# Kernel optimization log

Measured on AMD Instinct MI355X. Metric: run time of the kernel, lower is better.

Reference implementation:

```python
import jax, jax.numpy as jnp
import numpy as np

T = 2048      # tokens (flattened batch*seq)
HID = 2048    # hidden_size
H = 16        # num heads
D = HID // H  # head_dim = 128
EPS = 1e-5
THETA = 1000000.0


def setup_inputs() -> dict:
    key = jax.random.key(0)
    k0, k1, k2 = jax.random.split(key, 3)
    return {
        "hidden_states": jax.random.normal(k0, (T, HID), jnp.float32),
        "positions": jnp.arange(T, dtype=jnp.int32),
        "w_qkv": jax.random.normal(k1, (HID, 3 * HID), jnp.float32) * 0.02,
        "q_norm_w": jnp.ones((HID,), jnp.float32),
        "k_norm_w": jnp.ones((HID,), jnp.float32),
        "w_o": jax.random.normal(k2, (HID, HID), jnp.float32) * 0.02,
    }


def _rmsnorm(x, w):
    # RMSNorm over the full flat q/k vector (q_size / kv_size), as in forward_native
    var = jnp.mean(jnp.square(x.astype(jnp.float32)), axis=-1, keepdims=True)
    return (x.astype(jnp.float32) * jax.lax.rsqrt(var + EPS)).astype(x.dtype) * w


def _rope(x, positions):
    # NEOX-style rotary over full head_dim. x: [T, H, D]
    half = D // 2
    inv_freq = 1.0 / (THETA ** (jnp.arange(half, dtype=jnp.float32) / half))
    ang = positions.astype(jnp.float32)[:, None] * inv_freq  # [T, half]
    cos = jnp.cos(ang)[:, None, :]  # [T, 1, half]
    sin = jnp.sin(ang)[:, None, :]
    x1, x2 = x[..., :half], x[..., half:]
    return jnp.concatenate([x1 * cos - x2 * sin, x2 * cos + x1 * sin], axis=-1)


def reference(hidden_states, positions, w_qkv, q_norm_w, k_norm_w, w_o):
    qkv = hidden_states @ w_qkv                      # [T, 3*HID]
    q, k, v = jnp.split(qkv, [HID, 2 * HID], axis=-1)
    q = _rmsnorm(q, q_norm_w)
    k = _rmsnorm(k, k_norm_w)
    q = _rope(q.reshape(T, H, D), positions)
    k = _rope(k.reshape(T, H, D), positions)
    v = v.reshape(T, H, D)
    scale = D ** -0.5
    scores = jnp.einsum('qhd,khd->hqk', q, k) * scale   # [H, T, T]
    causal = jnp.tril(jnp.ones((T, T), bool))
    scores = jnp.where(causal[None], scores, jnp.finfo(scores.dtype).min)
    probs = jax.nn.softmax(scores, axis=-1)
    attn = jnp.einsum('hqk,khd->qhd', probs, v).reshape(T, HID)
    return attn @ w_o
```

## Files before the change

kernel.cpp:

```cpp
#include <hip/hip_runtime.h>
#include <hip/hip_bf16.h>

typedef __attribute__((ext_vector_type(8))) short bf16x8;
typedef __attribute__((ext_vector_type(4))) float f32x4;

__device__ inline unsigned short f2b(float x) {
  __hip_bfloat16 b = __float2bfloat16(x);
  return *reinterpret_cast<unsigned short*>(&b);
}
__device__ inline float b2f(unsigned short u) {
  return __bfloat162float(*reinterpret_cast<const __hip_bfloat16*>(&u));
}

#define GAS(p) ((const __attribute__((address_space(1))) void*)(p))
#define LAS(p) ((__attribute__((address_space(3))) void*)(p))

__global__ __launch_bounds__(256) void cast_f32_bf16(const float* __restrict__ X,
                                                     unsigned short* __restrict__ Y, int n4) {
  int i = blockIdx.x * 256 + threadIdx.x;
  if (i < n4) {
    float4 v = reinterpret_cast<const float4*>(X)[i];
    ushort4 o;
    o.x = f2b(v.x); o.y = f2b(v.y); o.z = f2b(v.z); o.w = f2b(v.w);
    reinterpret_cast<ushort4*>(Y)[i] = o;
  }
}

__global__ __launch_bounds__(256) void tcast(const float* __restrict__ W,
                                             unsigned short* __restrict__ Wt, int K, int N) {
  __shared__ float tile[32][33];
  int n0 = blockIdx.x * 32, k0 = blockIdx.y * 32;
  int tx = threadIdx.x & 31, ty = threadIdx.x >> 5;
#pragma unroll
  for (int i = 0; i < 32; i += 8)
    tile[ty + i][tx] = W[(size_t)(k0 + ty + i) * N + n0 + tx];
  __syncthreads();
#pragma unroll
  for (int i = 0; i < 32; i += 8)
    Wt[(size_t)(n0 + ty + i) * K + k0 + tx] = f2b(tile[tx][ty + i]);
}

__global__ __launch_bounds__(256) void vtrans(const float* __restrict__ qkv,
                                              unsigned short* __restrict__ Vt) {
  __shared__ unsigned short tile[32][33];
  int c0 = blockIdx.x * 32;
  int t0 = blockIdx.y * 32;
  int tx = threadIdx.x & 31, ty = threadIdx.x >> 5;
#pragma unroll
  for (int i = 0; i < 32; i += 8)
    tile[ty + i][tx] = f2b(qkv[(size_t)(t0 + ty + i) * 6144 + 4096 + c0 + tx]);
  __syncthreads();
#pragma unroll
  for (int i = 0; i < 32; i += 8)
    Vt[(size_t)(c0 + ty + i) * 2048 + t0 + tx] = tile[tx][ty + i];
}

__global__ __launch_bounds__(256) void gemm_bt(const unsigned short* __restrict__ A,
                                               const unsigned short* __restrict__ Bt,
                                               float* __restrict__ C, int M, int N, int K) {
  __shared__ unsigned short As[128 * 32];
  __shared__ unsigned short Bs[128 * 32];
  const int tid = threadIdx.x;
  const int w = tid >> 6, l = tid & 63;
  const int lr = l & 15, lg = l >> 4;
  const int wm = (w >> 1) << 6, wn = (w & 1) << 6;
  const size_t bm = (size_t)blockIdx.y * 128, bn = (size_t)blockIdx.x * 128;

  const int srow = tid >> 2;
  const int scol = (tid & 3) << 3;
  const unsigned short* Ag = A + (bm + srow) * (size_t)K + scol;
  const unsigned short* Bg = Bt + (bn + srow) * (size_t)K + scol;
  unsigned short* Al = As + w * 512;
  unsigned short* Bl = Bs + w * 512;

  f32x4 acc[4][4] = {};

  for (int k0 = 0; k0 < K; k0 += 32) {
    __syncthreads();
    __builtin_amdgcn_global_load_lds(GAS(Ag + k0), LAS(Al), 16, 0, 0);
    __builtin_amdgcn_global_load_lds(GAS(Ag + (size_t)64 * K + k0), LAS(Al + 2048), 16, 0, 0);
    __builtin_amdgcn_global_load_lds(GAS(Bg + k0), LAS(Bl), 16, 0, 0);
    __builtin_amdgcn_global_load_lds(GAS(Bg + (size_t)64 * K + k0), LAS(Bl + 2048), 16, 0, 0);
    __syncthreads();

    bf16x8 af[4], bfr[4];
#pragma unroll
    for (int mi = 0; mi < 4; ++mi)
      af[mi] = *reinterpret_cast<const bf16x8*>(&As[(wm + mi * 16 + lr) * 32 + lg * 8]);
#pragma unroll
    for (int ni = 0; ni < 4; ++ni)
      bfr[ni] = *reinterpret_cast<const bf16x8*>(&Bs[(wn + ni * 16 + lr) * 32 + lg * 8]);
#pragma unroll
    for (int mi = 0; mi < 4; ++mi)
#pragma unroll
      for (int ni = 0; ni < 4; ++ni)
        acc[mi][ni] = __builtin_amdgcn_mfma_f32_16x16x32_bf16(af[mi], bfr[ni], acc[mi][ni], 0, 0, 0);
  }

#pragma unroll
  for (int mi = 0; mi < 4; ++mi)
#pragma unroll
    for (int ni = 0; ni < 4; ++ni)
#pragma unroll
      for (int r = 0; r < 4; ++r) {
        size_t row = bm + wm + mi * 16 + lg * 4 + r;
        size_t col = bn + wn + ni * 16 + lr;
        C[row * N + col] = acc[mi][ni][r];
      }
}

__global__ __launch_bounds__(256) void rms_rope(const float* __restrict__ qkv,
                                                const int* __restrict__ pos,
                                                const float* __restrict__ qw,
                                                const float* __restrict__ kw,
                                                unsigned short* __restrict__ qb,
                                                unsigned short* __restrict__ kb) {
  const int t = blockIdx.x;
  const float* row = qkv + (size_t)t * 6144;
  __shared__ float redq[4], redk[4];
  __shared__ float cs[64], sn[64];
  const int tid = threadIdx.x, w = tid >> 6, l = tid & 63;

  float sq = 0.f, sk = 0.f;
#pragma unroll
  for (int i = 0; i < 8; ++i) {
    float a = row[tid + i * 256]; sq += a * a;
    float b = row[2048 + tid + i * 256]; sk += b * b;
  }
#pragma unroll
  for (int m = 32; m >= 1; m >>= 1) { sq += __shfl_xor(sq, m, 64); sk += __shfl_xor(sk, m, 64); }
  if (l == 0) { redq[w] = sq; redk[w] = sk; }
  if (tid < 64) {
    float fr = exp2f(-(float)tid * 0.31143075889569016f);
    float ang = (float)pos[t] * fr;
    cs[tid] = cosf(ang);
    sn[tid] = sinf(ang);
  }
  __syncthreads();
  float rq = rsqrtf((redq[0] + redq[1] + redq[2] + redq[3]) * (1.f / 2048.f) + 1e-5f);
  float rk = rsqrtf((redk[0] + redk[1] + redk[2] + redk[3]) * (1.f / 2048.f) + 1e-5f);

  unsigned short* qo = qb + (size_t)t * 2048;
  unsigned short* ko = kb + (size_t)t * 2048;
#pragma unroll
  for (int pp = 0; pp < 4; ++pp) {
    int pr = tid + pp * 256;
    int h = pr >> 6, j = pr & 63;
    int b0 = h * 128 + j;
    float c = cs[j], s = sn[j];
    float x1 = row[b0] * rq * qw[b0];
    float x2 = row[b0 + 64] * rq * qw[b0 + 64];
    qo[b0]      = f2b(x1 * c - x2 * s);
    qo[b0 + 64] = f2b(x2 * c + x1 * s);
    float y1 = row[2048 + b0] * rk * kw[b0];
    float y2 = row[2048 + b0 + 64] * rk * kw[b0 + 64];
    ko[b0]      = f2b(y1 * c - y2 * s);
    ko[b0 + 64] = f2b(y2 * c + y1 * s);
  }
}

__global__ __launch_bounds__(256) void attn_part(const unsigned short* __restrict__ qb,
                                                 const unsigned short* __restrict__ kb,
                                                 const unsigned short* __restrict__ vt,
                                                 unsigned short* __restrict__ Op,
                                                 float* __restrict__ ml) {
  __shared__ unsigned short Ks[64 * 128];
  __shared__ unsigned short Vs[128 * 64];
  __shared__ unsigned short Ps[4][16 * 72];
  const int qt = blockIdx.x, h = blockIdx.y, sp = blockIdx.z;
  const int q0 = qt * 64;
  const int kbeg = sp * 512;
  if (kbeg >= q0 + 64) return;
  const int kend = min(kbeg + 512, q0 + 64);
  const int tid = threadIdx.x, w = tid >> 6, l = tid & 63;
  const int lr = l & 15, lg = l >> 4;
  const float scale = 0.08838834764831845f;

  bf16x8 qf[4];
  {
    const unsigned short* qp = qb + (size_t)(q0 + w * 16 + lr) * 2048 + h * 128;
#pragma unroll
    for (int kc = 0; kc < 4; ++kc)
      qf[kc] = *reinterpret_cast<const bf16x8*>(qp + kc * 32 + lg * 8);
  }
  f32x4 oacc[8] = {};
  float mrow[4], lrow[4];
#pragma unroll
  for (int r = 0; r < 4; ++r) { mrow[r] = -1e30f; lrow[r] = 0.f; }

  for (int k0 = kbeg; k0 < kend; k0 += 64) {
    __syncthreads();
    {
      const int r0 = l >> 4, cph = l & 15;
#pragma unroll
      for (int rb = 0; rb < 16; rb += 4) {
        int row = w * 16 + rb + r0;
        int clog = (cph & 8) | ((cph & 7) ^ (row & 7));
        const unsigned short* src = kb + (size_t)(k0 + row) * 2048 + h * 128 + clog * 8;
        __builtin_amdgcn_global_load_lds(GAS(src), LAS((char*)Ks + (w * 16 + rb) * 256), 16, 0, 0);
      }
      const int r0v = l >> 3, cpv = l & 7;
#pragma unroll
      for (int rb = 0; rb < 32; rb += 8) {
        int row = w * 32 + rb + r0v;
        int clog = cpv ^ (row & 7);
        const unsigned short* src = vt + (size_t)(h * 128 + row) * 2048 + k0 + clog * 8;
        __builtin_amdgcn_global_load_lds(GAS(src), LAS((char*)Vs + (w * 32 + rb) * 128), 16, 0, 0);
      }
    }
    __syncthreads();

    f32x4 s[4] = {};
#pragma unroll
    for (int kc = 0; kc < 4; ++kc)
#pragma unroll
      for (int cg = 0; cg < 4; ++cg) {
        int key = cg * 16 + lr;
        int c = 4 * kc + lg;
        int cswz = (c & 8) | ((c & 7) ^ (key & 7));
        bf16x8 kf = *reinterpret_cast<const bf16x8*>(&Ks[key * 128 + cswz * 8]);
        s[cg] = __builtin_amdgcn_mfma_f32_16x16x32_bf16(qf[kc], kf, s[cg], 0, 0, 0);
      }

#pragma unroll
    for (int r = 0; r < 4; ++r) {
      const int qr = q0 + w * 16 + lg * 4 + r;
      float pv[4]; bool msk[4];
      float mx = -1e30f;
#pragma unroll
      for (int cg = 0; cg < 4; ++cg) {
        msk[cg] = (k0 + cg * 16 + lr) > qr;
        float v = msk[cg] ? -1e30f : s[cg][r] * scale;
        pv[cg] = v;
        mx = fmaxf(mx, v);
      }
#pragma unroll
      for (int m = 8; m >= 1; m >>= 1) mx = fmaxf(mx, __shfl_xor(mx, m, 16));
      float mnew = fmaxf(mrow[r], mx);
      float corr = __expf(mrow[r] - mnew);
      float ps = 0.f;
#pragma unroll
      for (int cg = 0; cg < 4; ++cg) {
        float pe = msk[cg] ? 0.f : __expf(pv[cg] - mnew);
        pv[cg] = pe; ps += pe;
      }
#pragma unroll
      for (int m = 8; m >= 1; m >>= 1) ps += __shfl_xor(ps, m, 16);
      lrow[r] = lrow[r] * corr + ps;
      mrow[r] = mnew;
#pragma unroll
      for (int ni = 0; ni < 8; ++ni) oacc[ni][r] *= corr;
#pragma unroll
      for (int cg = 0; cg < 4; ++cg)
        Ps[w][(lg * 4 + r) * 72 + cg * 16 + lr] = f2b(pv[cg]);
    }

#pragma unroll
    for (int ks = 0; ks < 2; ++ks) {
      bf16x8 pf = *reinterpret_cast<const bf16x8*>(&Ps[w][lr * 72 + ks * 32 + lg * 8]);
#pragma unroll
      for (int ni = 0; ni < 8; ++ni) {
        int d = ni * 16 + lr;
        int c = ks * 4 + lg;
        int cswz = c ^ (d & 7);
        bf16x8 vf = *reinterpret_cast<const bf16x8*>(&Vs[d * 64 + cswz * 8]);
        oacc[ni] = __builtin_amdgcn_mfma_f32_16x16x32_bf16(pf, vf, oacc[ni], 0, 0, 0);
      }
    }
  }

  const size_t base = (((size_t)sp * 16 + h) * 32 + qt) * 64;
#pragma unroll
  for (int ni = 0; ni < 8; ++ni)
#pragma unroll
    for (int r = 0; r < 4; ++r)
      Op[(base + w * 16 + lg * 4 + r) * 128 + ni * 16 + lr] = f2b(oacc[ni][r]);
  if (lr == 0) {
#pragma unroll
    for (int r = 0; r < 4; ++r) {
      size_t mi = (base + w * 16 + lg * 4 + r) * 2;
      ml[mi] = mrow[r]; ml[mi + 1] = lrow[r];
    }
  }
}

__global__ __launch_bounds__(256) void attn_combine(const unsigned short* __restrict__ Op,
                                                    const float* __restrict__ ml,
                                                    unsigned short* __restrict__ ob) {
  const int qt = blockIdx.x, h = blockIdx.y;
  const int q0 = qt * 64;
  const int ns = q0 / 512 + 1;
  const int t = threadIdx.x;
  const int row = t >> 2, dp = (t & 3) * 32;

  float m_s[4], l_s[4];
  float M = -1e30f;
#pragma unroll
  for (int s = 0; s < 4; ++s) {
    if (s < ns) {
      size_t mi = ((((size_t)s * 16 + h) * 32 + qt) * 64 + row) * 2;
      m_s[s] = ml[mi]; l_s[s] = ml[mi + 1];
    } else { m_s[s] = -1e30f; l_s[s] = 0.f; }
    M = fmaxf(M, m_s[s]);
  }
  float L = 0.f, wgt[4];
#pragma unroll
  for (int s = 0; s < 4; ++s) { wgt[s] = __expf(m_s[s] - M); L += l_s[s] * wgt[s]; }
  float invL = 1.f / L;

  float acc[32];
#pragma unroll
  for (int j = 0; j < 32; ++j) acc[j] = 0.f;
#pragma unroll
  for (int s = 0; s < 4; ++s) {
    if (s < ns) {
      const unsigned short* op = Op + ((((size_t)s * 16 + h) * 32 + qt) * 64 + row) * 128 + dp;
      float wg = wgt[s] * invL;
#pragma unroll
      for (int j = 0; j < 32; j += 8) {
        bf16x8 v = *reinterpret_cast<const bf16x8*>(op + j);
#pragma unroll
        for (int e = 0; e < 8; ++e) acc[j + e] += wg * b2f((unsigned short)v[e]);
      }
    }
  }
  unsigned short* o = ob + (size_t)(q0 + row) * 2048 + h * 128 + dp;
#pragma unroll
  for (int j = 0; j < 32; ++j) o[j] = f2b(acc[j]);
}

extern "C" void kernel_launch(void* const* d_in, const int* in_sizes, int n_in,
                              void* d_out, int out_size, void* d_ws, size_t ws_size,
                              hipStream_t stream) {
  const float* hs   = (const float*)d_in[0];
  const int*   pos  = (const int*)d_in[1];
  const float* wqkv = (const float*)d_in[2];
  const float* qnw  = (const float*)d_in[3];
  const float* knw  = (const float*)d_in[4];
  const float* wo   = (const float*)d_in[5];
  float* out = (float*)d_out;

  char* ws = (char*)d_ws;
  size_t off = 0;
  auto take = [&](size_t bytes) {
    char* p = ws + off;
    off = (off + bytes + 255) & ~(size_t)255;
    return p;
  };
  unsigned short* hidA  = (unsigned short*)take(2048ull * 2048 * 2);
  unsigned short* wqkvT = (unsigned short*)take(6144ull * 2048 * 2);
  unsigned short* woT   = (unsigned short*)take(2048ull * 2048 * 2);
  float*          qkvF  = (float*)take(2048ull * 6144 * 4);
  unsigned short* qbv   = (unsigned short*)take(2048ull * 2048 * 2);
  unsigned short* kbv   = (unsigned short*)take(2048ull * 2048 * 2);
  unsigned short* vtb   = (unsigned short*)take(2048ull * 2048 * 2);
  unsigned short* attnb = (unsigned short*)take(2048ull * 2048 * 2);
  unsigned short* Opart = (unsigned short*)qkvF;
  float*          mlb   = (float*)((char*)qkvF + 32ull * 1024 * 1024);

  cast_f32_bf16<<<4096, 256, 0, stream>>>(hs, hidA, 1048576);
  tcast<<<dim3(192, 64), 256, 0, stream>>>(wqkv, wqkvT, 2048, 6144);
  tcast<<<dim3(64, 64), 256, 0, stream>>>(wo, woT, 2048, 2048);
  gemm_bt<<<dim3(48, 16), 256, 0, stream>>>(hidA, wqkvT, qkvF, 2048, 6144, 2048);
  rms_rope<<<2048, 256, 0, stream>>>(qkvF, pos, qnw, knw, qbv, kbv);
  vtrans<<<dim3(64, 64), 256, 0, stream>>>(qkvF, vtb);
  attn_part<<<dim3(32, 16, 4), 256, 0, stream>>>(qbv, kbv, vtb, Opart, mlb);
  attn_combine<<<dim3(32, 16), 256, 0, stream>>>(Opart, mlb, attnb);
  gemm_bt<<<dim3(16, 16), 256, 0, stream>>>(attnb, woT, out, 2048, 2048, 2048);
}
```

Baseline: 362.6 us.

## Split attention KV into finer chunks, skip masking on full tiles, fold scale into Q

The KV split length drops from 512 to 256, giving eight splits, and partial outputs are packed into a compact triangular layout so the combine step reads only the splits that exist. Tiles lying fully below the diagonal now run an unmasked path, and only the diagonal tile applies the causal mask. The softmax scale and log2(e) are folded into Q inside rms_rope, so the kernels use exp2f, and the row-sum reduction moves out of the loop to the end. MFMA sections get s_setprio hints. Finer splits improve load balance and occupancy across the causal triangle, at the cost of more partial writes and more combine work.

```diff
diff --git a/kernel.cpp b/kernel.cpp
--- a/kernel.cpp
+++ b/kernel.cpp
@@ -139,6 +139,7 @@
   __syncthreads();
   float rq = rsqrtf((redq[0] + redq[1] + redq[2] + redq[3]) * (1.f / 2048.f) + 1e-5f);
   float rk = rsqrtf((redk[0] + redk[1] + redk[2] + redk[3]) * (1.f / 2048.f) + 1e-5f);
+  const float rqs = rq * 0.12753102543609887f;
 
   unsigned short* qo = qb + (size_t)t * 2048;
   unsigned short* ko = kb + (size_t)t * 2048;
@@ -148,8 +149,8 @@
     int h = pr >> 6, j = pr & 63;
     int b0 = h * 128 + j;
     float c = cs[j], s = sn[j];
-    float x1 = row[b0] * rq * qw[b0];
-    float x2 = row[b0 + 64] * rq * qw[b0 + 64];
+    float x1 = row[b0] * rqs * qw[b0];
+    float x2 = row[b0 + 64] * rqs * qw[b0 + 64];
     qo[b0]      = f2b(x1 * c - x2 * s);
     qo[b0 + 64] = f2b(x2 * c + x1 * s);
     float y1 = row[2048 + b0] * rk * kw[b0];
@@ -157,6 +158,93 @@
     ko[b0]      = f2b(y1 * c - y2 * s);
     ko[b0 + 64] = f2b(y2 * c + y1 * s);
   }
+}
+
+__device__ __forceinline__ void stage_kv(const unsigned short* __restrict__ kb_h,
+                                         const unsigned short* __restrict__ vt_h,
+                                         int k0, int w, int l,
+                                         unsigned short* Ks, unsigned short* Vs) {
+  const int r0 = l >> 4, cph = l & 15;
+#pragma unroll
+  for (int rb = 0; rb < 16; rb += 4) {
+    int row = w * 16 + rb + r0;
+    int clog = (cph & 8) | ((cph & 7) ^ (row & 7));
+    const unsigned short* src = kb_h + (size_t)(k0 + row) * 2048 + clog * 8;
+    __builtin_amdgcn_global_load_lds(GAS(src), LAS((char*)Ks + (w * 16 + rb) * 256), 16, 0, 0);
+  }
+  const int r0v = l >> 3, cpv = l & 7;
+#pragma unroll
+  for (int rb = 0; rb < 32; rb += 8) {
+    int row = w * 32 + rb + r0v;
+    int clog = cpv ^ (row & 7);
+    const unsigned short* src = vt_h + (size_t)row * 2048 + k0 + clog * 8;
+    __builtin_amdgcn_global_load_lds(GAS(src), LAS((char*)Vs + (w * 32 + rb) * 128), 16, 0, 0);
+  }
+}
+
+template <bool MASKED>
+__device__ __forceinline__ void attn_tile(int k0, int qrbase, int lr, int lg,
+                                          const bf16x8 (&qf)[4],
+                                          const unsigned short* __restrict__ Ks,
+                                          const unsigned short* __restrict__ Vs,
+                                          unsigned short* __restrict__ PsW,
+                                          f32x4 (&oacc)[8], float (&mrow)[4], float (&lrow)[4]) {
+  f32x4 s[4] = {};
+  __builtin_amdgcn_s_setprio(1);
+#pragma unroll
+  for (int kc = 0; kc < 4; ++kc)
+#pragma unroll
+    for (int cg = 0; cg < 4; ++cg) {
+      int key = cg * 16 + lr;
+      int c = 4 * kc + lg;
+      int cswz = (c & 8) | ((c & 7) ^ (key & 7));
+      bf16x8 kf = *reinterpret_cast<const bf16x8*>(&Ks[key * 128 + cswz * 8]);
+      s[cg] = __builtin_amdgcn_mfma_f32_16x16x32_bf16(qf[kc], kf, s[cg], 0, 0, 0);
+    }
+  __builtin_amdgcn_s_setprio(0);
+
+#pragma unroll
+  for (int r = 0; r < 4; ++r) {
+    const int qr = qrbase + lg * 4 + r;
+    float p0 = s[0][r], p1 = s[1][r], p2 = s[2][r], p3 = s[3][r];
+    if (MASKED) {
+      if (k0 + lr > qr)      p0 = -1e30f;
+      if (k0 + 16 + lr > qr) p1 = -1e30f;
+      if (k0 + 32 + lr > qr) p2 = -1e30f;
+      if (k0 + 48 + lr > qr) p3 = -1e30f;
+    }
+    float mx = fmaxf(fmaxf(p0, p1), fmaxf(p2, p3));
+#pragma unroll
+    for (int m = 8; m >= 1; m >>= 1) mx = fmaxf(mx, __shfl_xor(mx, m, 16));
+    float mnew = fmaxf(mrow[r], mx);
+    float corr = exp2f(mrow[r] - mnew);
+    p0 = exp2f(p0 - mnew); p1 = exp2f(p1 - mnew);
+    p2 = exp2f(p2 - mnew); p3 = exp2f(p3 - mnew);
+    lrow[r] = lrow[r] * corr + ((p0 + p1) + (p2 + p3));
+    mrow[r] = mnew;
+#pragma unroll
+    for (int ni = 0; ni < 8; ++ni) oacc[ni][r] *= corr;
+    const int prow = (lg * 4 + r) * 72;
+    PsW[prow + lr]      = f2b(p0);
+    PsW[prow + 16 + lr] = f2b(p1);
+    PsW[prow + 32 + lr] = f2b(p2);
+    PsW[prow + 48 + lr] = f2b(p3);
+  }
+
+  __builtin_amdgcn_s_setprio(1);
+#pragma unroll
+  for (int ks = 0; ks < 2; ++ks) {
+    bf16x8 pf = *reinterpret_cast<const bf16x8*>(&PsW[lr * 72 + ks * 32 + lg * 8]);
+#pragma unroll
+    for (int ni = 0; ni < 8; ++ni) {
+      int d = ni * 16 + lr;
+      int c = ks * 4 + lg;
+      int cswz = c ^ (d & 7);
+      bf16x8 vf = *reinterpret_cast<const bf16x8*>(&Vs[d * 64 + cswz * 8]);
+      oacc[ni] = __builtin_amdgcn_mfma_f32_16x16x32_bf16(pf, vf, oacc[ni], 0, 0, 0);
+    }
+  }
+  __builtin_amdgcn_s_setprio(0);
 }
 
 __global__ __launch_bounds__(256) void attn_part(const unsigned short* __restrict__ qb,
@@ -169,16 +257,15 @@
   __shared__ unsigned short Ps[4][16 * 72];
   const int qt = blockIdx.x, h = blockIdx.y, sp = blockIdx.z;
   const int q0 = qt * 64;
-  const int kbeg = sp * 512;
+  const int kbeg = sp * 256;
   if (kbeg >= q0 + 64) return;
-  const int kend = min(kbeg + 512, q0 + 64);
   const int tid = threadIdx.x, w = tid >> 6, l = tid & 63;
   const int lr = l & 15, lg = l >> 4;
-  const float scale = 0.08838834764831845f;
+  const int qrbase = q0 + w * 16;
 
   bf16x8 qf[4];
   {
-    const unsigned short* qp = qb + (size_t)(q0 + w * 16 + lr) * 2048 + h * 128;
+    const unsigned short* qp = qb + (size_t)(qrbase + lr) * 2048 + h * 128;
 #pragma unroll
     for (int kc = 0; kc < 4; ++kc)
       qf[kc] = *reinterpret_cast<const bf16x8*>(qp + kc * 32 + lg * 8);
@@ -188,97 +275,40 @@
 #pragma unroll
   for (int r = 0; r < 4; ++r) { mrow[r] = -1e30f; lrow[r] = 0.f; }
 
-  for (int k0 = kbeg; k0 < kend; k0 += 64) {
-    __syncthreads();
-    {
-      const int r0 = l >> 4, cph = l & 15;
-#pragma unroll
-      for (int rb = 0; rb < 16; rb += 4) {
-        int row = w * 16 + rb + r0;
-        int clog = (cph & 8) | ((cph & 7) ^ (row & 7));
-        const unsigned short* src = kb + (size_t)(k0 + row) * 2048 + h * 128 + clog * 8;
-        __builtin_amdgcn_global_load_lds(GAS(src), LAS((char*)Ks + (w * 16 + rb) * 256), 16, 0, 0);
-      }
-      const int r0v = l >> 3, cpv = l & 7;
-#pragma unroll
-      for (int rb = 0; rb < 32; rb += 8) {
-        int row = w * 32 + rb + r0v;
-        int clog = cpv ^ (row & 7);
-        const unsigned short* src = vt + (size_t)(h * 128 + row) * 2048 + k0 + clog * 8;
-        __builtin_amdgcn_global_load_lds(GAS(src), LAS((char*)Vs + (w * 32 + rb) * 128), 16, 0, 0);
-      }
-    }
-    __syncthreads();
-
-    f32x4 s[4] = {};
-#pragma unroll
-    for (int kc = 0; kc < 4; ++kc)
-#pragma unroll
-      for (int cg = 0; cg < 4; ++cg) {
-        int key = cg * 16 + lr;
-        int c = 4 * kc + lg;
-        int cswz = (c & 8) | ((c & 7) ^ (key & 7));
-        bf16x8 kf = *reinterpret_cast<const bf16x8*>(&Ks[key * 128 + cswz * 8]);
-        s[cg] = __builtin_amdgcn_mfma_f32_16x16x32_bf16(qf[kc], kf, s[cg], 0, 0, 0);
-      }
-
+  const unsigned short* kb_h = kb + h * 128;
+  const unsigned short* vt_h = vt + (size_t)h * 128 * 2048;
+
+  const int kstop_full = min(kbeg + 256, q0);
+  for (int k0 = kbeg; k0 < kstop_full; k0 += 64) {
+    __syncthreads();
+    stage_kv(kb_h, vt_h, k0, w, l, Ks, Vs);
+    __syncthreads();
+    attn_tile<false>(k0, qrbase, lr, lg, qf, Ks, Vs, Ps[w], oacc, mrow, lrow);
+  }
+  if (q0 >= kbeg && q0 < kbeg + 256) {
+    __syncthreads();
+    stage_kv(kb_h, vt_h, q0, w, l, Ks, Vs);
+    __syncthreads();
+    attn_tile<true>(q0, qrbase, lr, lg, qf, Ks, Vs, Ps[w], oacc, mrow, lrow);
+  }
+
+#pragma unroll
+  for (int r = 0; r < 4; ++r)
+#pragma unroll
+    for (int m = 8; m >= 1; m >>= 1) lrow[r] += __shfl_xor(lrow[r], m, 16);
+
+  const int g = qt >> 2, j = qt & 3;
+  const size_t u = (size_t)h * 144 + (g + 1) * (2 * g + j) + sp;
+  const size_t baserow = u * 64 + w * 16;
+#pragma unroll
+  for (int ni = 0; ni < 8; ++ni)
+#pragma unroll
+    for (int r = 0; r < 4; ++r)
+      Op[(baserow + lg * 4 + r) * 128 + ni * 16 + lr] = f2b(oacc[ni][r]);
+  if (lr == 0) {
 #pragma unroll
     for (int r = 0; r < 4; ++r) {
-      const int qr = q0 + w * 16 + lg * 4 + r;
-      float pv[4]; bool msk[4];
-      float mx = -1e30f;
-#pragma unroll
-      for (int cg = 0; cg < 4; ++cg) {
-        msk[cg] = (k0 + cg * 16 + lr) > qr;
-        float v = msk[cg] ? -1e30f : s[cg][r] * scale;
-        pv[cg] = v;
-        mx = fmaxf(mx, v);
-      }
-#pragma unroll
-      for (int m = 8; m >= 1; m >>= 1) mx = fmaxf(mx, __shfl_xor(mx, m, 16));
-      float mnew = fmaxf(mrow[r], mx);
-      float corr = __expf(mrow[r] - mnew);
-      float ps = 0.f;
-#pragma unroll
-      for (int cg = 0; cg < 4; ++cg) {
-        float pe = msk[cg] ? 0.f : __expf(pv[cg] - mnew);
-        pv[cg] = pe; ps += pe;
-      }
-#pragma unroll
-      for (int m = 8; m >= 1; m >>= 1) ps += __shfl_xor(ps, m, 16);
-      lrow[r] = lrow[r] * corr + ps;
-      mrow[r] = mnew;
-#pragma unroll
-      for (int ni = 0; ni < 8; ++ni) oacc[ni][r] *= corr;
-#pragma unroll
-      for (int cg = 0; cg < 4; ++cg)
-        Ps[w][(lg * 4 + r) * 72 + cg * 16 + lr] = f2b(pv[cg]);
-    }
-
-#pragma unroll
-    for (int ks = 0; ks < 2; ++ks) {
-      bf16x8 pf = *reinterpret_cast<const bf16x8*>(&Ps[w][lr * 72 + ks * 32 + lg * 8]);
-#pragma unroll
-      for (int ni = 0; ni < 8; ++ni) {
-        int d = ni * 16 + lr;
-        int c = ks * 4 + lg;
-        int cswz = c ^ (d & 7);
-        bf16x8 vf = *reinterpret_cast<const bf16x8*>(&Vs[d * 64 + cswz * 8]);
-        oacc[ni] = __builtin_amdgcn_mfma_f32_16x16x32_bf16(pf, vf, oacc[ni], 0, 0, 0);
-      }
-    }
-  }
-
-  const size_t base = (((size_t)sp * 16 + h) * 32 + qt) * 64;
-#pragma unroll
-  for (int ni = 0; ni < 8; ++ni)
-#pragma unroll
-    for (int r = 0; r < 4; ++r)
-      Op[(base + w * 16 + lg * 4 + r) * 128 + ni * 16 + lr] = f2b(oacc[ni][r]);
-  if (lr == 0) {
-#pragma unroll
-    for (int r = 0; r < 4; ++r) {
-      size_t mi = (base + w * 16 + lg * 4 + r) * 2;
+      size_t mi = (baserow + lg * 4 + r) * 2;
       ml[mi] = mrow[r]; ml[mi + 1] = lrow[r];
     }
   }
@@ -289,44 +319,46 @@
                                                     unsigned short* __restrict__ ob) {
   const int qt = blockIdx.x, h = blockIdx.y;
   const int q0 = qt * 64;
-  const int ns = q0 / 512 + 1;
+  const int g = qt >> 2, j = qt & 3;
+  const int ns = g + 1;
+  const size_t ubase = (size_t)h * 144 + (g + 1) * (2 * g + j);
   const int t = threadIdx.x;
   const int row = t >> 2, dp = (t & 3) * 32;
 
-  float m_s[4], l_s[4];
+  float m_s[8], l_s[8];
   float M = -1e30f;
 #pragma unroll
-  for (int s = 0; s < 4; ++s) {
+  for (int s = 0; s < 8; ++s) {
     if (s < ns) {
-      size_t mi = ((((size_t)s * 16 + h) * 32 + qt) * 64 + row) * 2;
+      size_t mi = ((ubase + s) * 64 + row) * 2;
       m_s[s] = ml[mi]; l_s[s] = ml[mi + 1];
     } else { m_s[s] = -1e30f; l_s[s] = 0.f; }
     M = fmaxf(M, m_s[s]);
   }
-  float L = 0.f, wgt[4];
-#pragma unroll
-  for (int s = 0; s < 4; ++s) { wgt[s] = __expf(m_s[s] - M); L += l_s[s] * wgt[s]; }
+  float L = 0.f, wgt[8];
+#pragma unroll
+  for (int s = 0; s < 8; ++s) { wgt[s] = exp2f(m_s[s] - M); L += l_s[s] * wgt[s]; }
   float invL = 1.f / L;
 
   float acc[32];
 #pragma unroll
-  for (int j = 0; j < 32; ++j) acc[j] = 0.f;
-#pragma unroll
-  for (int s = 0; s < 4; ++s) {
+  for (int jj = 0; jj < 32; ++jj) acc[jj] = 0.f;
+#pragma unroll
+  for (int s = 0; s < 8; ++s) {
     if (s < ns) {
-      const unsigned short* op = Op + ((((size_t)s * 16 + h) * 32 + qt) * 64 + row) * 128 + dp;
+      const unsigned short* op = Op + ((ubase + s) * 64 + row) * 128 + dp;
       float wg = wgt[s] * invL;
 #pragma unroll
-      for (int j = 0; j < 32; j += 8) {
-        bf16x8 v = *reinterpret_cast<const bf16x8*>(op + j);
-#pragma unroll
-        for (int e = 0; e < 8; ++e) acc[j + e] += wg * b2f((unsigned short)v[e]);
+      for (int jj = 0; jj < 32; jj += 8) {
+        bf16x8 v = *reinterpret_cast<const bf16x8*>(op + jj);
+#pragma unroll
+        for (int e = 0; e < 8; ++e) acc[jj + e] += wg * b2f((unsigned short)v[e]);
       }
     }
   }
   unsigned short* o = ob + (size_t)(q0 + row) * 2048 + h * 128 + dp;
 #pragma unroll
-  for (int j = 0; j < 32; ++j) o[j] = f2b(acc[j]);
+  for (int jj = 0; jj < 32; ++jj) o[jj] = f2b(acc[jj]);
 }
 
 extern "C" void kernel_launch(void* const* d_in, const int* in_sizes, int n_in,
@@ -356,7 +388,7 @@
   unsigned short* vtb   = (unsigned short*)take(2048ull * 2048 * 2);
   unsigned short* attnb = (unsigned short*)take(2048ull * 2048 * 2);
   unsigned short* Opart = (unsigned short*)qkvF;
-  float*          mlb   = (float*)((char*)qkvF + 32ull * 1024 * 1024);
+  float*          mlb   = (float*)((char*)qkvF + 40ull * 1024 * 1024);
 
   cast_f32_bf16<<<4096, 256, 0, stream>>>(hs, hidA, 1048576);
   tcast<<<dim3(192, 64), 256, 0, stream>>>(wqkv, wqkvT, 2048, 6144);
@@ -364,7 +396,7 @@
   gemm_bt<<<dim3(48, 16), 256, 0, stream>>>(hidA, wqkvT, qkvF, 2048, 6144, 2048);
   rms_rope<<<2048, 256, 0, stream>>>(qkvF, pos, qnw, knw, qbv, kbv);
   vtrans<<<dim3(64, 64), 256, 0, stream>>>(qkvF, vtb);
-  attn_part<<<dim3(32, 16, 4), 256, 0, stream>>>(qbv, kbv, vtb, Opart, mlb);
+  attn_part<<<dim3(32, 16, 8), 256, 0, stream>>>(qbv, kbv, vtb, Opart, mlb);
   attn_combine<<<dim3(32, 16), 256, 0, stream>>>(Opart, mlb, attnb);
   gemm_bt<<<dim3(16, 16), 256, 0, stream>>>(attnb, woT, out, 2048, 2048, 2048);
 }
```

Result: slower. 374.7 us (+3.3%).
